# Performance work log

Hardware: AMD Instinct MI355X
Metric: run time of the kernel (lower is better)

## Reference

```python
import jax, jax.numpy as jnp
import numpy as np
import math

GRID_H, GRID_W = 128, 128
INIT_LENGTHSCALE = 0.1

def make_grid(h, w):
    yy, xx = jnp.meshgrid(jnp.arange(h, dtype=jnp.float32) / h,
                          jnp.arange(w, dtype=jnp.float32) / w, indexing='ij')
    return jnp.stack([xx, yy], axis=-1)  # [H, W, 2]

def setup_inputs() -> dict:
    key = jax.random.key(0)
    k1, k2 = jax.random.split(key)
    B, N, C = 8, 2048, 3
    return {
        'x_context': jax.random.uniform(k1, (B, N, 2), dtype=jnp.float32),
        'y_context': jax.random.normal(k2, (B, N, C), dtype=jnp.float32),
        'context_mask': jnp.ones((B, N), dtype=jnp.float32),
        'log_lengthscale': jnp.asarray(math.log(INIT_LENGTHSCALE), dtype=jnp.float32),
        'grid': make_grid(GRID_H, GRID_W),
    }

def reference(x_context, y_context, context_mask, log_lengthscale, grid):
    B = x_context.shape[0]
    H, W = grid.shape[0], grid.shape[1]
    grid_flat = grid.reshape(-1, 2)  # [HW, 2]
    # squared pairwise distances: [B, HW, N]
    sq_dist = jnp.sum((grid_flat[None, :, None, :] - x_context[:, None, :, :]) ** 2, axis=-1)
    lengthscale = jnp.exp(log_lengthscale)
    weights = jnp.exp(-0.5 * sq_dist / (lengthscale ** 2))
    weights = weights * context_mask[:, None, :]
    signal = jnp.einsum('bgn,bnc->bgc', weights, y_context)  # [B, HW, C]
    density = jnp.sum(weights, axis=-1, keepdims=True)        # [B, HW, 1]
    grid_repr = jnp.concatenate([signal, density], axis=-1).reshape(B, H, W, -1)
    return jnp.transpose(grid_repr, (0, 3, 1, 2))  # [B, C+1, H, W]
```

## Files before the change

kernel.cpp:

```cpp
#include <hip/hip_runtime.h>
#include <hip/hip_bf16.h>
#include <math.h>


typedef float f32x4 __attribute__((ext_vector_type(4)));
typedef short s16x8 __attribute__((ext_vector_type(8)));

constexpr int BB = 8, NN = 2048, GH = 128, GW = 128;
constexpr int GY_TILE = 16;
constexpr int KSPLIT  = 8;
constexpr int NK      = NN / KSPLIT;
constexpr int NCH     = NK / 32;
constexpr int OUTSZ   = BB * 4 * GH * GW;

__device__ __forceinline__ void split2(float v0, float v1,
                                       unsigned& hi, unsigned& lo) {
    __hip_bfloat16 a = __float2bfloat16(v0);
    __hip_bfloat16 b = __float2bfloat16(v1);
    float fa = __bfloat162float(a), fb = __bfloat162float(b);
    __hip_bfloat16 ra = __float2bfloat16(v0 - fa);
    __hip_bfloat16 rb = __float2bfloat16(v1 - fb);
    unsigned short ua, ub, uc, ud;
    __builtin_memcpy(&ua, &a, 2);  __builtin_memcpy(&ub, &b, 2);
    __builtin_memcpy(&uc, &ra, 2); __builtin_memcpy(&ud, &rb, 2);
    hi = (unsigned)ua | ((unsigned)ub << 16);
    lo = (unsigned)uc | ((unsigned)ud << 16);
}

template <bool ATOMIC>
__global__ __launch_bounds__(256, 2) void setconv_mfma(
    const float* __restrict__ xc,
    const float* __restrict__ yc,
    const float* __restrict__ mask,
    const float* __restrict__ logls,
    const float* __restrict__ grid,
    float* __restrict__ dst)
{
    __shared__ unsigned sA[2][4 * 64 * 4];
    __shared__ unsigned sB[2][8 * 64 * 4];

    const int ks  = blockIdx.x;
    const int gyt = blockIdx.y;
    const int b   = blockIdx.z;
    const int tid = threadIdx.x;
    const int l   = tid & 63;
    const int w   = tid >> 6;

    const float ls = __expf(logls[0]);
    const float cc = -0.72134752044f / (ls * ls);

    const int lane_s = tid >> 2;
    const int jp     = tid & 3;
    const int sb15   = lane_s & 15;
    const int kg     = lane_s >> 4;
    const int k0     = ((jp >> 1) << 4) | (kg << 2) | ((jp & 1) << 1);
    const int ch     = sb15 & 3;
    const int gyb    = sb15 >> 2;

    float gxv[8];
#pragma unroll
    for (int r = 0; r < 8; ++r) gxv[r] = grid[(r * 16 + sb15) * 2 + 0];
    float gyv[4];
#pragma unroll
    for (int r = 0; r < 4; ++r)
        gyv[r] = grid[(size_t)(gyt * GY_TILE + r * 4 + gyb) * GW * 2 + 1];

    const int mtb = (w & 1) * 2;
    const int ntb = (w >> 1) * 4;

    f32x4 acc[2][4];
#pragma unroll
    for (int i = 0; i < 2; ++i)
#pragma unroll
        for (int j = 0; j < 4; ++j) acc[i][j] = (f32x4){0.f, 0.f, 0.f, 0.f};

    const int nb0 = b * NN + ks * NK;

    for (int chn = 0; chn < NCH; ++chn) {
        const int kbase = nb0 + chn * 32 + k0;
        const float4 xy = *(const float4*)&xc[(size_t)kbase * 2];
        const float2 mk = *(const float2*)&mask[kbase];
        float yv0 = 0.f, yv1 = 0.f;
        if (ch < 3) {
            yv0 = yc[(size_t)kbase * 3 + ch];
            yv1 = yc[(size_t)(kbase + 1) * 3 + ch];
        }
        const float y40 = (ch < 3) ? yv0 * mk.x : mk.x;
        const float y41 = (ch < 3) ? yv1 * mk.y : mk.y;

        __syncthreads();

#pragma unroll
        for (int r = 0; r < 8; ++r) {
            float d0 = gxv[r] - xy.x, d1 = gxv[r] - xy.z;
            float v0 = exp2f(cc * d0 * d0), v1 = exp2f(cc * d1 * d1);
            unsigned hi, lo;
            split2(v0, v1, hi, lo);
            sB[0][r * 256 + tid] = hi;
            sB[1][r * 256 + tid] = lo;
        }
#pragma unroll
        for (int r = 0; r < 4; ++r) {
            float d0 = gyv[r] - xy.y, d1 = gyv[r] - xy.w;
            float e0 = exp2f(cc * d0 * d0) * y40;
            float e1 = exp2f(cc * d1 * d1) * y41;
            unsigned hi, lo;
            split2(e0, e1, hi, lo);
            sA[0][r * 256 + tid] = hi;
            sA[1][r * 256 + tid] = lo;
        }
        __syncthreads();

        const s16x8* pAh = (const s16x8*)sA[0];
        const s16x8* pAl = (const s16x8*)sA[1];
        const s16x8* pBh = (const s16x8*)sB[0];
        const s16x8* pBl = (const s16x8*)sB[1];
        s16x8 ah[2], al[2], bh[4], bl[4];
#pragma unroll
        for (int i = 0; i < 2; ++i) {
            ah[i] = pAh[(mtb + i) * 64 + l];
            al[i] = pAl[(mtb + i) * 64 + l];
        }
#pragma unroll
        for (int j = 0; j < 4; ++j) {
            bh[j] = pBh[(ntb + j) * 64 + l];
            bl[j] = pBl[(ntb + j) * 64 + l];
        }
#pragma unroll
        for (int i = 0; i < 2; ++i)
#pragma unroll
            for (int j = 0; j < 4; ++j) {
                acc[i][j] = __builtin_amdgcn_mfma_f32_16x16x32_bf16(
                    ah[i], bh[j], acc[i][j], 0, 0, 0);
                acc[i][j] = __builtin_amdgcn_mfma_f32_16x16x32_bf16(
                    ah[i], bl[j], acc[i][j], 0, 0, 0);
                acc[i][j] = __builtin_amdgcn_mfma_f32_16x16x32_bf16(
                    al[i], bh[j], acc[i][j], 0, 0, 0);
            }
    }

    const int colg = l & 15, rowg = l >> 4;
    float* slice = ATOMIC ? dst : dst + (size_t)ks * OUTSZ;
#pragma unroll
    for (int i = 0; i < 2; ++i) {
        const int gy = gyt * GY_TILE + (mtb + i) * 4 + rowg;
#pragma unroll
        for (int j = 0; j < 4; ++j) {
            const int gx = (ntb + j) * 16 + colg;
#pragma unroll
            for (int r = 0; r < 4; ++r) {
                const size_t off = (((size_t)(b * 4 + r)) * GH + gy) * GW + gx;
                if (ATOMIC) atomicAdd(&slice[off], acc[i][j][r]);
                else        slice[off] = acc[i][j][r];
            }
        }
    }
}

__global__ __launch_bounds__(256, 8) void setconv_reduce(
    const float* __restrict__ pw,
    float* __restrict__ out)
{
    const int n4 = OUTSZ / 4;
    const int stride = gridDim.x * 256;
    const float4* p = (const float4*)pw;
    for (int i = blockIdx.x * 256 + threadIdx.x; i < n4; i += stride) {
        float4 s = p[i];
#pragma unroll
        for (int k = 1; k < KSPLIT; ++k) {
            float4 v = p[(size_t)k * n4 + i];
            s.x += v.x; s.y += v.y; s.z += v.z; s.w += v.w;
        }
        ((float4*)out)[i] = s;
    }
}

extern "C" void kernel_launch(void* const* d_in, const int* in_sizes, int n_in,
                              void* d_out, int out_size, void* d_ws, size_t ws_size,
                              hipStream_t stream) {
    const float* xc    = (const float*)d_in[0];
    const float* yc    = (const float*)d_in[1];
    const float* mask  = (const float*)d_in[2];
    const float* logls = (const float*)d_in[3];
    const float* grid  = (const float*)d_in[4];
    float* out = (float*)d_out;

    dim3 gdim(KSPLIT, GH / GY_TILE, BB);
    const size_t need = (size_t)KSPLIT * OUTSZ * sizeof(float);

    if (ws_size >= need) {
        float* pw = (float*)d_ws;
        setconv_mfma<false><<<gdim, 256, 0, stream>>>(xc, yc, mask, logls,
                                                      grid, pw);
        setconv_reduce<<<dim3(512), 256, 0, stream>>>(pw, out);
    } else {
        hipMemsetAsync(out, 0, (size_t)out_size * sizeof(float), stream);
        setconv_mfma<true><<<gdim, 256, 0, stream>>>(xc, yc, mask, logls,
                                                     grid, out);
    }
}
```

Baseline: 89.43 us.

## Raise K-split to 16, prefetch next chunk, cut register pressure for higher occupancy

Makes the K-split a template parameter and uses 16 splits when the workspace allows, doubling the grid so more blocks fill the GPU. Launch bounds go from 2 to 4 blocks per SM, and the grid coordinates are reloaded inside the loop instead of held in registers, to reduce register pressure. The next chunk's context loads are issued before the barrier so they overlap the current chunk's work. B fragments are loaded one at a time inside the MFMA loop to shorten register live ranges. In exchange, the partial-sum workspace doubles and the reduce kernel reads twice as much data.

```diff
diff --git a/kernel.cpp b/kernel.cpp
--- a/kernel.cpp
+++ b/kernel.cpp
@@ -8,10 +8,7 @@
 
 constexpr int BB = 8, NN = 2048, GH = 128, GW = 128;
 constexpr int GY_TILE = 16;
-constexpr int KSPLIT  = 8;
-constexpr int NK      = NN / KSPLIT;
-constexpr int NCH     = NK / 32;
-constexpr int OUTSZ   = BB * 4 * GH * GW;
+constexpr int OUTSZ = BB * 4 * GH * GW;
 
 __device__ __forceinline__ void split2(float v0, float v1,
                                        unsigned& hi, unsigned& lo) {
@@ -27,8 +24,8 @@
     lo = (unsigned)uc | ((unsigned)ud << 16);
 }
 
-template <bool ATOMIC>
-__global__ __launch_bounds__(256, 2) void setconv_mfma(
+template <int KS, bool ATOMIC>
+__global__ __launch_bounds__(256, 4) void setconv_mfma(
     const float* __restrict__ xc,
     const float* __restrict__ yc,
     const float* __restrict__ mask,
@@ -36,6 +33,9 @@
     const float* __restrict__ grid,
     float* __restrict__ dst)
 {
+    constexpr int NK  = NN / KS;
+    constexpr int NCH = NK / 32;
+
     __shared__ unsigned sA[2][4 * 64 * 4];
     __shared__ unsigned sB[2][8 * 64 * 4];
 
@@ -57,14 +57,6 @@
     const int ch     = sb15 & 3;
     const int gyb    = sb15 >> 2;
 
-    float gxv[8];
-#pragma unroll
-    for (int r = 0; r < 8; ++r) gxv[r] = grid[(r * 16 + sb15) * 2 + 0];
-    float gyv[4];
-#pragma unroll
-    for (int r = 0; r < 4; ++r)
-        gyv[r] = grid[(size_t)(gyt * GY_TILE + r * 4 + gyb) * GW * 2 + 1];
-
     const int mtb = (w & 1) * 2;
     const int ntb = (w >> 1) * 4;
 
@@ -76,15 +68,16 @@
 
     const int nb0 = b * NN + ks * NK;
 
+    int kb = nb0 + k0;
+    float4 xy = *(const float4*)&xc[(size_t)kb * 2];
+    float2 mk = *(const float2*)&mask[kb];
+    float yv0 = 0.f, yv1 = 0.f;
+    if (ch < 3) {
+        yv0 = yc[(size_t)kb * 3 + ch];
+        yv1 = yc[(size_t)(kb + 1) * 3 + ch];
+    }
+
     for (int chn = 0; chn < NCH; ++chn) {
-        const int kbase = nb0 + chn * 32 + k0;
-        const float4 xy = *(const float4*)&xc[(size_t)kbase * 2];
-        const float2 mk = *(const float2*)&mask[kbase];
-        float yv0 = 0.f, yv1 = 0.f;
-        if (ch < 3) {
-            yv0 = yc[(size_t)kbase * 3 + ch];
-            yv1 = yc[(size_t)(kbase + 1) * 3 + ch];
-        }
         const float y40 = (ch < 3) ? yv0 * mk.x : mk.x;
         const float y41 = (ch < 3) ? yv1 * mk.y : mk.y;
 
@@ -92,22 +85,31 @@
 
 #pragma unroll
         for (int r = 0; r < 8; ++r) {
-            float d0 = gxv[r] - xy.x, d1 = gxv[r] - xy.z;
-            float v0 = exp2f(cc * d0 * d0), v1 = exp2f(cc * d1 * d1);
+            float gxv = grid[(r * 16 + sb15) * 2 + 0];
+            float d0 = gxv - xy.x, d1 = gxv - xy.z;
             unsigned hi, lo;
-            split2(v0, v1, hi, lo);
+            split2(exp2f(cc * d0 * d0), exp2f(cc * d1 * d1), hi, lo);
             sB[0][r * 256 + tid] = hi;
             sB[1][r * 256 + tid] = lo;
         }
 #pragma unroll
         for (int r = 0; r < 4; ++r) {
-            float d0 = gyv[r] - xy.y, d1 = gyv[r] - xy.w;
-            float e0 = exp2f(cc * d0 * d0) * y40;
-            float e1 = exp2f(cc * d1 * d1) * y41;
+            float gyv = grid[(size_t)(gyt * GY_TILE + r * 4 + gyb) * GW * 2 + 1];
+            float d0 = gyv - xy.y, d1 = gyv - xy.w;
             unsigned hi, lo;
-            split2(e0, e1, hi, lo);
+            split2(exp2f(cc * d0 * d0) * y40, exp2f(cc * d1 * d1) * y41, hi, lo);
             sA[0][r * 256 + tid] = hi;
             sA[1][r * 256 + tid] = lo;
+        }
+
+        if (chn + 1 < NCH) {
+            kb = nb0 + (chn + 1) * 32 + k0;
+            xy = *(const float4*)&xc[(size_t)kb * 2];
+            mk = *(const float2*)&mask[kb];
+            if (ch < 3) {
+                yv0 = yc[(size_t)kb * 3 + ch];
+                yv1 = yc[(size_t)(kb + 1) * 3 + ch];
+            }
         }
         __syncthreads();
 
@@ -115,7 +117,7 @@
         const s16x8* pAl = (const s16x8*)sA[1];
         const s16x8* pBh = (const s16x8*)sB[0];
         const s16x8* pBl = (const s16x8*)sB[1];
-        s16x8 ah[2], al[2], bh[4], bl[4];
+        s16x8 ah[2], al[2];
 #pragma unroll
         for (int i = 0; i < 2; ++i) {
             ah[i] = pAh[(mtb + i) * 64 + l];
@@ -123,20 +125,18 @@
         }
 #pragma unroll
         for (int j = 0; j < 4; ++j) {
-            bh[j] = pBh[(ntb + j) * 64 + l];
-            bl[j] = pBl[(ntb + j) * 64 + l];
-        }
-#pragma unroll
-        for (int i = 0; i < 2; ++i)
-#pragma unroll
-            for (int j = 0; j < 4; ++j) {
+            s16x8 bh = pBh[(ntb + j) * 64 + l];
+            s16x8 bl = pBl[(ntb + j) * 64 + l];
+#pragma unroll
+            for (int i = 0; i < 2; ++i) {
                 acc[i][j] = __builtin_amdgcn_mfma_f32_16x16x32_bf16(
-                    ah[i], bh[j], acc[i][j], 0, 0, 0);
+                    ah[i], bh, acc[i][j], 0, 0, 0);
                 acc[i][j] = __builtin_amdgcn_mfma_f32_16x16x32_bf16(
-                    ah[i], bl[j], acc[i][j], 0, 0, 0);
+                    ah[i], bl, acc[i][j], 0, 0, 0);
                 acc[i][j] = __builtin_amdgcn_mfma_f32_16x16x32_bf16(
-                    al[i], bh[j], acc[i][j], 0, 0, 0);
+                    al[i], bh, acc[i][j], 0, 0, 0);
             }
+        }
     }
 
     const int colg = l & 15, rowg = l >> 4;
@@ -157,6 +157,7 @@
     }
 }
 
+template <int KS>
 __global__ __launch_bounds__(256, 8) void setconv_reduce(
     const float* __restrict__ pw,
     float* __restrict__ out)
@@ -167,7 +168,7 @@
     for (int i = blockIdx.x * 256 + threadIdx.x; i < n4; i += stride) {
         float4 s = p[i];
 #pragma unroll
-        for (int k = 1; k < KSPLIT; ++k) {
+        for (int k = 1; k < KS; ++k) {
             float4 v = p[(size_t)k * n4 + i];
             s.x += v.x; s.y += v.y; s.z += v.z; s.w += v.w;
         }
@@ -185,17 +186,25 @@
     const float* grid  = (const float*)d_in[4];
     float* out = (float*)d_out;
 
-    dim3 gdim(KSPLIT, GH / GY_TILE, BB);
-    const size_t need = (size_t)KSPLIT * OUTSZ * sizeof(float);
-
-    if (ws_size >= need) {
+    const size_t need16 = (size_t)16 * OUTSZ * sizeof(float);
+    const size_t need8  = (size_t)8  * OUTSZ * sizeof(float);
+
+    if (ws_size >= need16) {
         float* pw = (float*)d_ws;
-        setconv_mfma<false><<<gdim, 256, 0, stream>>>(xc, yc, mask, logls,
-                                                      grid, pw);
-        setconv_reduce<<<dim3(512), 256, 0, stream>>>(pw, out);
+        dim3 gdim(16, GH / GY_TILE, BB);
+        setconv_mfma<16, false><<<gdim, 256, 0, stream>>>(xc, yc, mask, logls,
+                                                          grid, pw);
+        setconv_reduce<16><<<dim3(512), 256, 0, stream>>>(pw, out);
+    } else if (ws_size >= need8) {
+        float* pw = (float*)d_ws;
+        dim3 gdim(8, GH / GY_TILE, BB);
+        setconv_mfma<8, false><<<gdim, 256, 0, stream>>>(xc, yc, mask, logls,
+                                                         grid, pw);
+        setconv_reduce<8><<<dim3(512), 256, 0, stream>>>(pw, out);
     } else {
         hipMemsetAsync(out, 0, (size_t)out_size * sizeof(float), stream);
-        setconv_mfma<true><<<gdim, 256, 0, stream>>>(xc, yc, mask, logls,
-                                                     grid, out);
-    }
-}
+        dim3 gdim(8, GH / GY_TILE, BB);
+        setconv_mfma<8, true><<<gdim, 256, 0, stream>>>(xc, yc, mask, logls,
+                                                        grid, out);
+    }
+}
```

Result: slower. 91.53 us (+2.4%).
